# Optimization experiments

Hardware: AMD Instinct MI355X
Metric: run time of the kernel (lower is better)

Reference implementation:

```python
import jax, jax.numpy as jnp
import numpy as np

B = 64        # graphs per batch
N_PER = 1024  # nodes per graph (equal-size graphs -> to_dense_batch mask is all-true)
C = 128       # in_channels
K = 64        # pooled clusters (k)
DEG = 32      # average degree
N = B * N_PER
E = N * DEG


def setup_inputs() -> dict:
    key = jax.random.key(0)
    k1, k2, k3, k4, k5 = jax.random.split(key, 5)
    x = jax.random.normal(k1, (N, C), dtype=jnp.float32)
    # edges constrained to stay within each graph (PyG batched-graph invariant)
    src_l = jax.random.randint(k2, (B, N_PER * DEG), 0, N_PER)
    dst_l = jax.random.randint(k3, (B, N_PER * DEG), 0, N_PER)
    off = (jnp.arange(B) * N_PER)[:, None]
    edge_index = jnp.stack([(src_l + off).reshape(-1), (dst_l + off).reshape(-1)], axis=0)
    batch = jnp.repeat(jnp.arange(B), N_PER)
    W_msg = jax.random.normal(k4, (C, K), dtype=jnp.float32) / np.float32(np.sqrt(C))
    W_root = jax.random.normal(k5, (C, K), dtype=jnp.float32) / np.float32(np.sqrt(C))
    b = jnp.zeros((K,), dtype=jnp.float32)
    return {"x": x, "edge_index": edge_index, "batch": batch,
            "W_msg": W_msg, "W_root": W_root, "b": b}


def reference(x, edge_index, batch, W_msg, W_root, b):
    src, dst = edge_index[0], edge_index[1]
    # ---- LSSMP: learned-score message passing -> cluster scores s [N, K] ----
    m = jax.nn.elu(x @ W_msg)                                  # per-node messages [N, K]
    agg = jax.ops.segment_sum(m[src], dst, num_segments=N)     # scatter-add over edges
    s = jnp.tanh(agg + x @ W_root + b)                         # act = tanh
    # ---- to_dense_batch (equal-size graphs: pure reshape, mask all-true) ----
    xd = x.reshape(B, N_PER, C)
    sd = s.reshape(B, N_PER, K)
    # ---- to_dense_adj ----
    g = src // N_PER
    adj = jnp.zeros((B, N_PER, N_PER), jnp.float32).at[g, src % N_PER, dst % N_PER].add(1.0)
    # ---- dense_connect: S = softmax(s); out = S^T X ; out_adj = S^T A S ----
    S = jax.nn.softmax(sd, axis=-1)                            # [B, N_PER, K]
    out = jnp.einsum('bnk,bnc->bkc', S, xd)                    # [B, K, C]
    out_adj = jnp.einsum('bkn,bnm,bml->bkl',
                         S.transpose(0, 2, 1), adj, S)         # [B, K, K]
    # ---- to_sparse_batch: pooled adjacency is dense -> all-pairs edges ----
    x_out = out.reshape(B * K, C)
    grid = jnp.stack(jnp.meshgrid(jnp.arange(K), jnp.arange(K), indexing='ij'), 0).reshape(2, -1)
    offs = (jnp.arange(B) * K)[None, :, None]
    edge_index_out = (grid[:, None, :] + offs).reshape(2, -1)  # [2, B*K*K]
    batch_out = jnp.repeat(jnp.arange(B), K)
    # original returns (x, edge_index, None, batch, None, None); adj values are dropped
    del out_adj
    return x_out, edge_index_out, batch_out
```

## Files before the change

kernel.cpp:

```cpp
#include <hip/hip_runtime.h>
#include <hip/hip_bf16.h>

typedef __hip_bfloat16 bf16;

#define NPER 1024
#define CC   128
#define KK   64
#define NTOT 65536
#define ETOT 2097152
#define EPG  32768
#define ESL  8192

#define M_OFF    0
#define R_OFF    8388608
#define SORT_OFF 16777216
#define RP_OFF   20971520
#define FLAG_OFF 21233664
#define ZB_OFF   21233728
#define WS_NEED  21233984ULL
#define WF_OFF   21233984
#define WS_NEED2 21266752ULL
#define GH_OFF   M_OFF
#define GC_OFF   (M_OFF + 2097152)

typedef short bf16x8 __attribute__((ext_vector_type(8)));
typedef _Float16 half8 __attribute__((ext_vector_type(8)));
typedef float f32x4 __attribute__((ext_vector_type(4)));

__device__ __forceinline__ float t15_rb(float v) {
    return __bfloat162float(__float2bfloat16(v));
}
__device__ __forceinline__ float t15_bf(unsigned short h) {
    unsigned int w = ((unsigned int)h) << 16;
    float f;
    __builtin_memcpy(&f, &w, 4);
    return f;
}
__device__ __forceinline__ unsigned short t15_f2b(float f) {
    bf16 h = __float2bfloat16(f);
    unsigned short u;
    __builtin_memcpy(&u, &h, 2);
    return u;
}

__device__ __forceinline__ int t15_src(const int* ei, int e, int mode) {
    return (mode == 2 ? ei[2 * e] : ei[e]) & 65535;
}
__device__ __forceinline__ int t15_dst(const int* ei, int e, int mode) {
    return (mode == 2 ? ei[2 * ETOT + 2 * e] : ei[ETOT + e]) & 65535;
}

__global__ __launch_bounds__(1024) void t15_hist(const int* __restrict__ ei,
                                                 int* __restrict__ ghist,
                                                 const float* __restrict__ Wm,
                                                 const float* __restrict__ Wr,
                                                 unsigned short* __restrict__ wf) {
    int t = threadIdx.x;
    int blk = blockIdx.x;
    if (blk == 256) {
        if (!wf) return;
        for (int idx = t; idx < 16384; idx += 1024) {
            int w = idx >> 13;
            int r = idx & 8191;
            int fr = r >> 3;
            int j = r & 7;
            int lane = fr & 63;
            int sc = fr >> 6;
            int step = sc >> 2, ct = sc & 3;
            int c = step * 32 + 8 * (lane >> 4) + j;
            int kk = ct * 16 + (lane & 15);
            const float* W = w ? Wr : Wm;
            wf[idx] = t15_f2b(W[c * 64 + kk]);
        }
        return;
    }
    __shared__ int hist[2048];
    __shared__ int sdet[1024];
    __shared__ int smode;
    int ebase = blk * ESL;
    sdet[t] = ei[2 * (ebase + t) + 1];
    __syncthreads();
    for (int off = 512; off; off >>= 1) {
        if (t < off) sdet[t] |= sdet[t + off];
        __syncthreads();
    }
    if (t == 0) smode = (sdet[0] != 0) ? 1 : 2;
    hist[t] = 0;
    hist[t + 1024] = 0;
    __syncthreads();
    int mode = smode;
    for (int i = t; i < ESL; i += 1024) {
        int e = ebase + i;
        int s = t15_src(ei, e, mode) & (NPER - 1);
        int d = t15_dst(ei, e, mode) & (NPER - 1);
        atomicAdd(&hist[(d << 1) | ((s >> 9) & 1)], 1);
    }
    __syncthreads();
    ghist[blk * 2048 + t] = hist[t];
    ghist[blk * 2048 + 1024 + t] = hist[t + 1024];
}

__global__ __launch_bounds__(1024) void t15_scan(const int* __restrict__ ghist,
                                                 int* __restrict__ gcur,
                                                 unsigned short* __restrict__ rowptr,
                                                 float* __restrict__ zbias) {
    __shared__ int sh[8192];
    __shared__ int sscan[1024];
    int t = threadIdx.x, g = blockIdx.x;
    if (g == 0 && t < 64) zbias[t] = 0.f;
    for (int i = t; i < 8192; i += 1024) sh[i] = ghist[g * 8192 + i];
    __syncthreads();
    int b0 = 2 * t, b1 = 2 * t + 1;
    int h0[4], h1[4];
    int c0 = 0, c1 = 0;
#pragma unroll
    for (int q = 0; q < 4; ++q) {
        h0[q] = sh[q * 2048 + b0]; c0 += h0[q];
        h1[q] = sh[q * 2048 + b1]; c1 += h1[q];
    }
    int ts = c0 + c1;
    sscan[t] = ts;
    __syncthreads();
    for (int off = 1; off < 1024; off <<= 1) {
        int v = sscan[t];
        int a = (t >= off) ? sscan[t - off] : 0;
        __syncthreads();
        sscan[t] = v + a;
        __syncthreads();
    }
    int incl = sscan[t], excl = incl - ts;
    rowptr[g * 2048 + b0] = (unsigned short)(excl + c0);
    rowptr[g * 2048 + b1] = (unsigned short)incl;
    int r0 = excl, r1 = excl + c0;
#pragma unroll
    for (int q = 0; q < 4; ++q) {
        gcur[(g * 4 + q) * 2048 + b0] = r0; r0 += h0[q];
        gcur[(g * 4 + q) * 2048 + b1] = r1; r1 += h1[q];
    }
}

__global__ __launch_bounds__(1024) void t15_scat(const int* __restrict__ ei,
                                                 const int* __restrict__ gcur,
                                                 unsigned short* __restrict__ sorted) {
    __shared__ int cur[2048];
    __shared__ int sdet[1024];
    __shared__ int smode;
    int t = threadIdx.x, blk = blockIdx.x;
    int ebase = blk * ESL;
    int g = blk >> 2;
    sdet[t] = ei[2 * (ebase + t) + 1];
    __syncthreads();
    for (int off = 512; off; off >>= 1) {
        if (t < off) sdet[t] |= sdet[t + off];
        __syncthreads();
    }
    if (t == 0) smode = (sdet[0] != 0) ? 1 : 2;
    cur[t] = gcur[blk * 2048 + t];
    cur[t + 1024] = gcur[blk * 2048 + 1024 + t];
    __syncthreads();
    int mode = smode;
    unsigned short* sg = sorted + g * EPG;
    for (int i = t; i < ESL; i += 1024) {
        int e = ebase + i;
        int s = t15_src(ei, e, mode) & (NPER - 1);
        int d = t15_dst(ei, e, mode) & (NPER - 1);
        int pos = atomicAdd(&cur[(d << 1) | ((s >> 9) & 1)], 1);
        if ((unsigned)pos < (unsigned)EPG) sg[pos] = (unsigned short)s;
    }
}

__global__ __launch_bounds__(256) void t15_mroot_mfma(
        const float* __restrict__ x, const unsigned short* __restrict__ wf,
        const float* __restrict__ bias,
        bf16* __restrict__ m_out, bf16* __restrict__ root_out) {
    __shared__ unsigned short sX[64 * CC];
    int t = threadIdx.x;
    int lane = t & 63;
    int wv = t >> 6;
    int ww = wv & 1;
    int ct0 = (wv >> 1) * 2;
    int rl = lane & 15, g2 = lane >> 4;

    bf16x8 bq[4][2];
    const uint4* wfq = (const uint4*)wf;
#pragma unroll
    for (int step = 0; step < 4; ++step)
#pragma unroll
        for (int cti = 0; cti < 2; ++cti) {
            uint4 u = wfq[(size_t)(((ww * 4 + step) * 4) + ct0 + cti) * 64 + lane];
            bq[step][cti] = __builtin_bit_cast(bf16x8, u);
        }
    float bv0 = bias[ct0 * 16 + rl];
    float bv1 = bias[ct0 * 16 + 16 + rl];
    bf16* dst = ww ? root_out : m_out;

    for (int ti = 0; ti < 2; ++ti) {
        int tile = blockIdx.x * 2 + ti;
        size_t rowbase = (size_t)tile * 64;
        if (ti) __syncthreads();
        const float4* xg = (const float4*)(x + rowbase * CC);
        for (int i = t; i < 2048; i += 256) {
            float4 v = xg[i];
            int row = i >> 5;
            int cb = (i & 31) * 8;
            int addr = row * 256 + (cb ^ ((row & 7) << 4));
            ushort4 h;
            h.x = t15_f2b(v.x); h.y = t15_f2b(v.y);
            h.z = t15_f2b(v.z); h.w = t15_f2b(v.w);
            *(ushort4*)((char*)sX + addr) = h;
        }
        __syncthreads();

        for (int rt = 0; rt < 4; ++rt) {
            int row = rt * 16 + rl;
            bf16x8 af[4];
#pragma unroll
            for (int step = 0; step < 4; ++step) {
                int addr = row * 256 + ((g2 * 16 + step * 64) ^ ((row & 7) << 4));
                uint4 u = *(const uint4*)((const char*)sX + addr);
                af[step] = __builtin_bit_cast(bf16x8, u);
            }
            f32x4 acc0 = {0.f, 0.f, 0.f, 0.f};
            f32x4 acc1 = {0.f, 0.f, 0.f, 0.f};
#pragma unroll
            for (int step = 0; step < 4; ++step) {
                acc0 = __builtin_amdgcn_mfma_f32_16x16x32_bf16(af[step], bq[step][0], acc0, 0, 0, 0);
                acc1 = __builtin_amdgcn_mfma_f32_16x16x32_bf16(af[step], bq[step][1], acc1, 0, 0, 0);
            }
            int n0 = (int)rowbase + rt * 16 + g2 * 4;
#pragma unroll
            for (int cti = 0; cti < 2; ++cti) {
                f32x4 a = cti ? acc1 : acc0;
                float bv = cti ? bv1 : bv0;
                int kk = (ct0 + cti) * 16 + rl;
#pragma unroll
                for (int r = 0; r < 4; ++r) {
                    float v = a[r];
                    if (ww) v += bv;
                    else    v = v > 0.f ? v : expm1f(v);
                    dst[(size_t)(n0 + r) * KK + kk] = __float2bfloat16(v);
                }
            }
        }
    }
}

__global__ void t15_mroot(const float* __restrict__ x, const float* __restrict__ Wm,
                          const float* __restrict__ Wr, const float* __restrict__ bias,
                          bf16* __restrict__ m_out, bf16* __restrict__ root_out) {
    __shared__ bf16 sWm[CC * KK];
    __shared__ bf16 sWr[CC * KK];
    __shared__ bf16 sX[64 * CC];
    int t = threadIdx.x;
    int nb = blockIdx.x * 64;
    for (int i = t; i < CC * KK; i += 256) {
        sWm[i] = __float2bfloat16(Wm[i]);
        sWr[i] = __float2bfloat16(Wr[i]);
    }
    const float4* xg = (const float4*)(x + (size_t)nb * CC);
    for (int i = t; i < (64 * CC) / 4; i += 256) {
        float4 v = xg[i];
        sX[i * 4 + 0] = __float2bfloat16(v.x);
        sX[i * 4 + 1] = __float2bfloat16(v.y);
        sX[i * 4 + 2] = __float2bfloat16(v.z);
        sX[i * 4 + 3] = __float2bfloat16(v.w);
    }
    int k = t & 63, rg = t >> 6;
    float bv = bias[k];
    __syncthreads();
    float accm[16], accr[16];
#pragma unroll
    for (int r = 0; r < 16; ++r) { accm[r] = 0.f; accr[r] = 0.f; }
    for (int c = 0; c < CC; ++c) {
        float wm = __bfloat162float(sWm[c * KK + k]);
        float wr = __bfloat162float(sWr[c * KK + k]);
#pragma unroll
        for (int r = 0; r < 16; ++r) {
            float xv = __bfloat162float(sX[(rg + 4 * r) * CC + c]);
            accm[r] += xv * wm;
            accr[r] += xv * wr;
        }
    }
#pragma unroll
    for (int r = 0; r < 16; ++r) {
        int n = nb + rg + 4 * r;
        float mv = accm[r];
        mv = mv > 0.f ? mv : expm1f(mv);
        m_out[(size_t)n * KK + k] = __float2bfloat16(mv);
        root_out[(size_t)n * KK + k] = __float2bfloat16(accr[r] + bv);
    }
}

__global__ __launch_bounds__(1024, 8) void t15_gatherlds(
        const unsigned short* __restrict__ rowptr,
        const unsigned short* __restrict__ sorted_src,
        const unsigned short* __restrict__ m_in,
        bf16* __restrict__ rootS) {
    __shared__ unsigned short sM[512 * KK];
    const unsigned* sM32 = (const unsigned*)sM;
    int lane = threadIdx.x & 63;
    int wv = threadIdx.x >> 6;
    int g = blockIdx.x >> 3;
    int nl0 = (blockIdx.x & 7) * 128 + wv * 8;
    int nbase = g * NPER + nl0;
    const unsigned short* rp = rowptr + g * 2048;
    const unsigned short* idx = sorted_src + g * EPG;
    int b0 = 2 * nl0;
    int l31 = lane & 31;
    bool hi = lane >= 32;

    unsigned rpv = 0;
    if (lane <= 16 && (b0 + lane) > 0) rpv = (unsigned)rp[b0 + lane - 1];

    float accL[8], accH[8];
    const unsigned* rS32 = (const unsigned*)rootS;
#pragma unroll
    for (int nn = 0; nn < 8; ++nn) {
        unsigned pr = rS32[(size_t)(nbase + nn) * 32 + l31];
        if (hi) pr = 0;
        accL[nn] = t15_bf((unsigned short)(pr & 0xffffu));
        accH[nn] = t15_bf((unsigned short)(pr >> 16));
    }

#pragma unroll
    for (int h = 0; h < 2; ++h) {
        unsigned vi[8];
#pragma unroll
        for (int nn = 0; nn < 8; ++nn) {
            int bb = 2 * nn + h;
            int s = (int)__builtin_amdgcn_readlane(rpv, bb);
            int e = (int)__builtin_amdgcn_readlane(rpv, bb + 1);
            if (s > EPG) s = EPG;
            if (e < s) e = s;
            if (e > EPG) e = EPG;
            int w0 = s >> 1;
            int wc = ((e + 1) >> 1) - w0;
            if (wc > 64) wc = 64;
            unsigned v = 0;
            if (lane < wc) v = *(const unsigned*)(idx + 2 * (w0 + lane));
            vi[nn] = v;
        }
        if (h) __syncthreads();
        const uint4* mg = (const uint4*)(m_in + ((size_t)g * NPER + h * 512) * KK);
        uint4* ml = (uint4*)sM;
        for (int i = threadIdx.x; i < (512 * KK) / 8; i += 1024) ml[i] = mg[i];
        __syncthreads();

#pragma unroll
        for (int nn = 0; nn < 8; ++nn) {
            int bb = 2 * nn + h;
            int s = (int)__builtin_amdgcn_readlane(rpv, bb);
            int e = (int)__builtin_amdgcn_readlane(rpv, bb + 1);
            if (s > EPG) s = EPG;
            if (e < s) e = s;
            if (e > EPG) e = EPG;
            int w0 = s >> 1;
            int wc = ((e + 1) >> 1) - w0;
            if (wc > 64) wc = 64;
            int elim = 2 * (w0 + wc);
            if (elim > e) elim = e;
            float aL = accL[nn], aH = accH[nn];
            int j = 0;
            if ((s & 1) && s < elim) {
                unsigned w = __builtin_amdgcn_readlane(vi[nn], 0);
                unsigned v = sM32[((w >> 16) & 511u) * 32 + l31];
                if (hi) v = 0;
                aL += t15_bf((unsigned short)(v & 0xffffu));
                aH += t15_bf((unsigned short)(v >> 16));
                j = 1;
            }
            int jfull = (elim >> 1) - w0;
            for (; j < jfull; ++j) {
                unsigned w = __builtin_amdgcn_readlane(vi[nn], j);
                unsigned s0 = w & 511u;
                unsigned s1 = (w >> 16) & 511u;
                unsigned sel = hi ? s1 : s0;
                unsigned v = sM32[sel * 32 + l31];
                aL += t15_bf((unsigned short)(v & 0xffffu));
                aH += t15_bf((unsigned short)(v >> 16));
            }
            if ((elim & 1) && elim > s) {
                unsigned w = __builtin_amdgcn_readlane(vi[nn], jfull);
                unsigned v = sM32[(w & 511u) * 32 + l31];
                if (hi) v = 0;
                aL += t15_bf((unsigned short)(v & 0xffffu));
                aH += t15_bf((unsigned short)(v >> 16));
            }
            for (int i = elim; i < e; ++i) {
                unsigned sv = __builtin_amdgcn_readfirstlane((unsigned)idx[i]);
                unsigned v = sM32[(sv & 511u) * 32 + l31];
                if (hi) v = 0;
                aL += t15_bf((unsigned short)(v & 0xffffu));
                aH += t15_bf((unsigned short)(v >> 16));
            }
            accL[nn] = aL; accH[nn] = aH;
        }
    }

#pragma unroll
    for (int nn = 0; nn < 8; ++nn) {
        float aL = accL[nn] + __shfl_xor(accL[nn], 32, 64);
        float aH = accH[nn] + __shfl_xor(accH[nn], 32, 64);
        float svL = tanhf(aL), svH = tanhf(aH);
        float mx = fmaxf(svL, svH);
        for (int o = 16; o; o >>= 1) mx = fmaxf(mx, __shfl_xor(mx, o, 64));
        float eL = expf(svL - mx), eH = expf(svH - mx);
        float sm = eL + eH;
        for (int o = 16; o; o >>= 1) sm += __shfl_xor(sm, o, 64);
        unsigned outw = (unsigned)t15_f2b(eL / sm) | ((unsigned)t15_f2b(eH / sm) << 16);
        if (lane < 32)
            ((unsigned*)rootS)[(size_t)(nbase + nn) * 32 + l31] = outw;
    }
}

__global__ __launch_bounds__(512) void t15_pool_mfma(
        const float* __restrict__ x, const bf16* __restrict__ S_in,
        float* __restrict__ outp) {
    __shared__ char sP[24576];
    int tt = threadIdx.x;
    if (blockIdx.x >= 256) {
        int gid = (blockIdx.x - 256) * 512 + tt;
        if (gid >= 528384) return;
        float val;
        if (gid < 524288) {
            int r = gid >> 18;
            int rem = gid & 262143;
            int b = rem >> 12;
            int p = rem & 4095;
            int v = (r == 0) ? (p >> 6) : (p & 63);
            val = (float)(v + b * 64);
        } else {
            val = (float)((gid - 524288) >> 6);
        }
        outp[524288 + gid] = t15_rb(val);
        return;
    }
    int lane = tt & 63;
    int wv = tt >> 6;
    int mt = wv & 3;
    int nt = wv >> 2;
    int rl = lane & 15, g2 = lane >> 4;
    int g = blockIdx.x >> 2;
    int cq = (blockIdx.x & 3) * 32;

    f32x4 acc = {0.f, 0.f, 0.f, 0.f};

    for (int tile = 0; tile < 8; ++tile) {
        size_t nbase = (size_t)g * NPER + tile * 128;
        if (tile) __syncthreads();
        const uint2* sg = (const uint2*)(S_in + nbase * KK);
        for (int i = 0; i < 4; ++i) {
            int idx = tt + 512 * i;
            int r = idx >> 4;
            int q = idx & 15;
            uint2 u = sg[idx];
            unsigned short b[4] = {(unsigned short)(u.x & 0xffff),
                                   (unsigned short)(u.x >> 16),
                                   (unsigned short)(u.y & 0xffff),
                                   (unsigned short)(u.y >> 16)};
#pragma unroll
            for (int j = 0; j < 4; ++j) {
                int k = 4 * q + j;
                _Float16 h = (_Float16)t15_bf(b[j]);
                *(_Float16*)(sP + k * 256 + ((2 * r) ^ ((k & 7) << 4))) = h;
            }
        }
        const float* xb = x + nbase * CC + cq;
        for (int i = 0; i < 2; ++i) {
            int idx = tt + 512 * i;
            int r = idx >> 3;
            int q = idx & 7;
            float4 v = *(const float4*)(xb + (size_t)r * CC + 4 * q);
#pragma unroll
            for (int j = 0; j < 4; ++j) {
                int c = 4 * q + j;
                float fv = (j == 0) ? v.x : (j == 1) ? v.y : (j == 2) ? v.z : v.w;
                _Float16 h = (_Float16)fv;
                *(_Float16*)(sP + 16384 + c * 256 + ((2 * r) ^ ((c & 7) << 4))) = h;
            }
        }
        __syncthreads();
#pragma unroll
        for (int ks = 0; ks < 4; ++ks) {
            int nb2 = 2 * (32 * ks + 8 * g2);
            int arow = 16 * mt + rl;
            uint4 ua = *(const uint4*)(sP + arow * 256 + (nb2 ^ ((arow & 7) << 4)));
            int brow = 16 * nt + rl;
            uint4 ub = *(const uint4*)(sP + 16384 + brow * 256 + (nb2 ^ ((brow & 7) << 4)));
            half8 A = __builtin_bit_cast(half8, ua);
            half8 B = __builtin_bit_cast(half8, ub);
            acc = __builtin_amdgcn_mfma_f32_16x16x32_f16(A, B, acc, 0, 0, 0);
        }
    }

#pragma unroll
    for (int r = 0; r < 4; ++r) {
        int krow = 16 * mt + 4 * g2 + r;
        outp[(size_t)(g * KK + krow) * CC + cq + 16 * nt + rl] = t15_rb(acc[r]);
    }
}

__global__ void t15_edgefill(float* __restrict__ outp) {
    int gid = blockIdx.x * 256 + threadIdx.x;
    if (gid >= 528384) return;
    float val;
    if (gid < 524288) {
        int r = gid >> 18;
        int rem = gid & 262143;
        int b = rem >> 12;
        int p = rem & 4095;
        int v = (r == 0) ? (p >> 6) : (p & 63);
        val = (float)(v + b * 64);
    } else {
        val = (float)((gid - 524288) >> 6);
    }
    outp[524288 + gid] = t15_rb(val);
}

extern "C" void kernel_launch(void* const* d_in, const int* in_sizes, int n_in,
                              void* d_out, int out_size, void* d_ws, size_t ws_size,
                              hipStream_t stream) {
    const float* x = nullptr; const int* ei = nullptr;
    const float* Wm = nullptr; const float* Wr = nullptr; const float* bias = nullptr;
    for (int i = 0; i < n_in; ++i) {
        int s = in_sizes[i];
        if (s == 8388608 && !x)       x  = (const float*)d_in[i];
        else if (s == 4194304 && !ei) ei = (const int*)d_in[i];
        else if (s == 8192) { if (!Wm) Wm = (const float*)d_in[i]; else if (!Wr) Wr = (const float*)d_in[i]; }
        else if (s == 64 && !bias)    bias = (const float*)d_in[i];
    }
    if (!x)  x  = (const float*)d_in[0];
    if (!ei) ei = (const int*)d_in[1];
    if (!Wm && n_in > 3) Wm = (const float*)d_in[3];
    if (!Wr && n_in > 4) Wr = (const float*)d_in[4];

    float* outp = (float*)d_out;
    bool out_ok = (out_size >= 1052672);
    bool ws_ok  = (ws_size >= WS_NEED) && x && ei && Wm && Wr;
    bool wf_ok  = (ws_size >= WS_NEED2);

    if (out_ok && !ws_ok) {
        t15_edgefill<<<2064, 256, 0, stream>>>(outp);
    }
    if (out_ok && ws_ok) {
        char* ws = (char*)d_ws;
        bf16*           m_buf  = (bf16*)(ws + M_OFF);
        bf16*           rootS  = (bf16*)(ws + R_OFF);
        unsigned short* sorted = (unsigned short*)(ws + SORT_OFF);
        unsigned short* rowptr = (unsigned short*)(ws + RP_OFF);
        float*          zbias  = (float*)(ws + ZB_OFF);
        unsigned short* wf     = wf_ok ? (unsigned short*)(ws + WF_OFF) : nullptr;
        int*            ghist  = (int*)(ws + GH_OFF);
        int*            gcur   = (int*)(ws + GC_OFF);
        const float* bz = bias ? bias : zbias;

        t15_hist<<<257, 1024, 0, stream>>>(ei, ghist, Wm, Wr, wf);
        t15_scan<<<64, 1024, 0, stream>>>(ghist, gcur, rowptr, zbias);
        t15_scat<<<256, 1024, 0, stream>>>(ei, gcur, sorted);
        if (wf_ok)
            t15_mroot_mfma<<<512, 256, 0, stream>>>(x, wf, bz, m_buf, rootS);
        else
            t15_mroot<<<NTOT / 64, 256, 0, stream>>>(x, Wm, Wr, bz, m_buf, rootS);
        t15_gatherlds<<<512, 1024, 0, stream>>>(rowptr, sorted,
                                                (const unsigned short*)m_buf, rootS);
        t15_pool_mfma<<<1288, 512, 0, stream>>>(x, rootS, outp);
    }
}
```

Baseline: 192.0 us.

## Compact edge keys in hist, LDS-local sort in scatter, new LDS swizzle

The histogram kernel now writes a packed 32-bit (dst,src) key per edge to workspace. The scatter kernel reads these compact keys instead of re-reading the 64-bit edge_index and re-detecting its layout. It then sorts locally in LDS via a per-block scan and copies contiguous runs out to global memory, so global writes are no longer scattered. Separately, the pooling kernel's LDS XOR swizzle uses a different slot function to reduce bank conflicts. The costs are an extra workspace write/read and serial per-bucket copy loops that may be unbalanced across threads.

```diff
diff --git a/kernel.cpp b/kernel.cpp
--- a/kernel.cpp
+++ b/kernel.cpp
@@ -22,6 +22,7 @@
 #define WS_NEED2 21266752ULL
 #define GH_OFF   M_OFF
 #define GC_OFF   (M_OFF + 2097152)
+#define KC_OFF   R_OFF
 
 typedef short bf16x8 __attribute__((ext_vector_type(8)));
 typedef _Float16 half8 __attribute__((ext_vector_type(8)));
@@ -50,8 +51,13 @@
     return (mode == 2 ? ei[2 * ETOT + 2 * e] : ei[ETOT + e]) & 65535;
 }
 
+__device__ __forceinline__ int t15_slot(int k) {
+    return ((k >> 2) & 7) | ((k & 1) << 3);
+}
+
 __global__ __launch_bounds__(1024) void t15_hist(const int* __restrict__ ei,
                                                  int* __restrict__ ghist,
+                                                 unsigned* __restrict__ kc,
                                                  const float* __restrict__ Wm,
                                                  const float* __restrict__ Wr,
                                                  unsigned short* __restrict__ wf) {
@@ -89,10 +95,12 @@
     hist[t + 1024] = 0;
     __syncthreads();
     int mode = smode;
+    unsigned* kcs = kc + ebase;
     for (int i = t; i < ESL; i += 1024) {
         int e = ebase + i;
         int s = t15_src(ei, e, mode) & (NPER - 1);
         int d = t15_dst(ei, e, mode) & (NPER - 1);
+        kcs[i] = ((unsigned)d << 10) | (unsigned)s;
         atomicAdd(&hist[(d << 1) | ((s >> 9) & 1)], 1);
     }
     __syncthreads();
@@ -139,33 +147,53 @@
     }
 }
 
-__global__ __launch_bounds__(1024) void t15_scat(const int* __restrict__ ei,
+__global__ __launch_bounds__(1024) void t15_scat(const unsigned* __restrict__ kc,
+                                                 const int* __restrict__ ghist,
                                                  const int* __restrict__ gcur,
                                                  unsigned short* __restrict__ sorted) {
-    __shared__ int cur[2048];
-    __shared__ int sdet[1024];
-    __shared__ int smode;
+    __shared__ unsigned short sBuf[ESL];
+    __shared__ int lofs[2048];
+    __shared__ int sscan[1024];
     int t = threadIdx.x, blk = blockIdx.x;
-    int ebase = blk * ESL;
     int g = blk >> 2;
-    sdet[t] = ei[2 * (ebase + t) + 1];
-    __syncthreads();
-    for (int off = 512; off; off >>= 1) {
-        if (t < off) sdet[t] |= sdet[t + off];
-        __syncthreads();
-    }
-    if (t == 0) smode = (sdet[0] != 0) ? 1 : 2;
-    cur[t] = gcur[blk * 2048 + t];
-    cur[t + 1024] = gcur[blk * 2048 + 1024 + t];
-    __syncthreads();
-    int mode = smode;
+    int b0 = 2 * t, b1 = 2 * t + 1;
+    int h0 = ghist[blk * 2048 + b0];
+    int h1 = ghist[blk * 2048 + b1];
+    int ts = h0 + h1;
+    sscan[t] = ts;
+    __syncthreads();
+    for (int off = 1; off < 1024; off <<= 1) {
+        int v = sscan[t];
+        int a = (t >= off) ? sscan[t - off] : 0;
+        __syncthreads();
+        sscan[t] = v + a;
+        __syncthreads();
+    }
+    int incl = sscan[t], excl = incl - ts;
+    lofs[b0] = excl;
+    lofs[b1] = excl + h0;
+    __syncthreads();
+    const unsigned* kcs = kc + blk * ESL;
+    for (int i = t; i < ESL; i += 1024) {
+        unsigned v = kcs[i];
+        int s = (int)(v & 1023u);
+        int d = (int)(v >> 10);
+        int pos = atomicAdd(&lofs[(d << 1) | ((s >> 9) & 1)], 1);
+        if ((unsigned)pos < (unsigned)ESL) sBuf[pos] = (unsigned short)s;
+    }
+    __syncthreads();
     unsigned short* sg = sorted + g * EPG;
-    for (int i = t; i < ESL; i += 1024) {
-        int e = ebase + i;
-        int s = t15_src(ei, e, mode) & (NPER - 1);
-        int d = t15_dst(ei, e, mode) & (NPER - 1);
-        int pos = atomicAdd(&cur[(d << 1) | ((s >> 9) & 1)], 1);
-        if ((unsigned)pos < (unsigned)EPG) sg[pos] = (unsigned short)s;
+    int le0 = lofs[b0] - h0;
+    int le1 = lofs[b1] - h1;
+    int gd0 = gcur[blk * 2048 + b0];
+    int gd1 = gcur[blk * 2048 + b1];
+    for (int j = 0; j < h0; ++j) {
+        int p = gd0 + j;
+        if ((unsigned)p < (unsigned)EPG) sg[p] = sBuf[le0 + j];
+    }
+    for (int j = 0; j < h1; ++j) {
+        int p = gd1 + j;
+        if ((unsigned)p < (unsigned)EPG) sg[p] = sBuf[le1 + j];
     }
 }
 
@@ -462,7 +490,7 @@
             for (int j = 0; j < 4; ++j) {
                 int k = 4 * q + j;
                 _Float16 h = (_Float16)t15_bf(b[j]);
-                *(_Float16*)(sP + k * 256 + ((2 * r) ^ ((k & 7) << 4))) = h;
+                *(_Float16*)(sP + k * 256 + ((2 * r) ^ (t15_slot(k) << 4))) = h;
             }
         }
         const float* xb = x + nbase * CC + cq;
@@ -476,7 +504,7 @@
                 int c = 4 * q + j;
                 float fv = (j == 0) ? v.x : (j == 1) ? v.y : (j == 2) ? v.z : v.w;
                 _Float16 h = (_Float16)fv;
-                *(_Float16*)(sP + 16384 + c * 256 + ((2 * r) ^ ((c & 7) << 4))) = h;
+                *(_Float16*)(sP + 16384 + c * 256 + ((2 * r) ^ (t15_slot(c) << 4))) = h;
             }
         }
         __syncthreads();
@@ -484,9 +512,9 @@
         for (int ks = 0; ks < 4; ++ks) {
             int nb2 = 2 * (32 * ks + 8 * g2);
             int arow = 16 * mt + rl;
-            uint4 ua = *(const uint4*)(sP + arow * 256 + (nb2 ^ ((arow & 7) << 4)));
+            uint4 ua = *(const uint4*)(sP + arow * 256 + (nb2 ^ (t15_slot(arow) << 4)));
             int brow = 16 * nt + rl;
-            uint4 ub = *(const uint4*)(sP + 16384 + brow * 256 + (nb2 ^ ((brow & 7) << 4)));
+            uint4 ub = *(const uint4*)(sP + 16384 + brow * 256 + (nb2 ^ (t15_slot(brow) << 4)));
             half8 A = __builtin_bit_cast(half8, ua);
             half8 B = __builtin_bit_cast(half8, ub);
             acc = __builtin_amdgcn_mfma_f32_16x16x32_f16(A, B, acc, 0, 0, 0);
@@ -552,11 +580,12 @@
         unsigned short* wf     = wf_ok ? (unsigned short*)(ws + WF_OFF) : nullptr;
         int*            ghist  = (int*)(ws + GH_OFF);
         int*            gcur   = (int*)(ws + GC_OFF);
+        unsigned*       kc     = (unsigned*)(ws + KC_OFF);
         const float* bz = bias ? bias : zbias;
 
-        t15_hist<<<257, 1024, 0, stream>>>(ei, ghist, Wm, Wr, wf);
+        t15_hist<<<257, 1024, 0, stream>>>(ei, ghist, kc, Wm, Wr, wf);
         t15_scan<<<64, 1024, 0, stream>>>(ghist, gcur, rowptr, zbias);
-        t15_scat<<<256, 1024, 0, stream>>>(ei, gcur, sorted);
+        t15_scat<<<256, 1024, 0, stream>>>(kc, ghist, gcur, sorted);
         if (wf_ok)
             t15_mroot_mfma<<<512, 256, 0, stream>>>(x, wf, bz, m_buf, rootS);
         else
```

Result: no change. 193.7 us (+0.9%).
